# Kernel optimization log

Measured on AMD Instinct MI355X. Metric: run time of the kernel, lower is better.

The kernel has to match this reference:

```python
import jax, jax.numpy as jnp
import numpy as np

VOCAB = 100000
DIM = 128
BATCH = 65536
N_NEG = 10


def setup_inputs() -> dict:
    key = jax.random.key(0)
    k1, k2, k3, k4, k5 = jax.random.split(key, 5)
    return {
        "pos_u": jax.random.randint(k1, (BATCH,), 0, VOCAB),
        "pos_v": jax.random.randint(k2, (BATCH,), 0, VOCAB),
        "neg_v": jax.random.randint(k3, (BATCH, N_NEG), 0, VOCAB),
        "u_weight": 0.01 * jax.random.normal(k4, (VOCAB, DIM), dtype=jnp.float32),
        "v_weight": 0.01 * jax.random.normal(k5, (VOCAB, DIM), dtype=jnp.float32),
    }


def reference(pos_u, pos_v, neg_v, u_weight, v_weight):
    emb_u = u_weight[pos_u]            # [B, D]
    emb_v = v_weight[pos_v]            # [B, D]
    emb_neg_v = v_weight[neg_v]        # [B, N, D]

    score = jnp.sum(emb_u * emb_v, axis=1)
    score = jnp.clip(score, -10.0, 10.0)
    score = -jax.nn.log_sigmoid(score)           # [B]

    neg_dots = jnp.einsum("bd,bnd->bn", emb_u, emb_neg_v)  # [B, N]
    # NOTE: faithful to source: neg term is ADDED (not negated) to the loss
    neg_score = jnp.sum(jax.nn.log_sigmoid(-neg_dots), axis=1)  # [B]

    return jnp.mean(score + neg_score)
```

## Files before the change

### kernel.cpp

```cpp
#include <hip/hip_runtime.h>
#include <hip/hip_fp8.h>

#define VOCAB 100000
#define DIM 128
#define BATCH 65536
#define N_NEG 10

#define BLOCKS (BATCH / 32)
#define QSCALE 256.0f
#define QINV   (1.0f / (256.0f * 256.0f))

__device__ __forceinline__ unsigned int pack4_fp8(float a, float b, float c, float d) {
    unsigned int r =  (unsigned int)__hip_fp8_e4m3(a).__x;
    r |= (unsigned int)__hip_fp8_e4m3(b).__x << 8;
    r |= (unsigned int)__hip_fp8_e4m3(c).__x << 16;
    r |= (unsigned int)__hip_fp8_e4m3(d).__x << 24;
    return r;
}

__device__ __forceinline__ float fp8_to_f(unsigned int b) {
    __hip_fp8_e4m3 t; t.__x = (__hip_fp8_storage_t)b; return (float)t;
}

__device__ __forceinline__ float dot16_fp8(uint4 w, const float* uf) {
    float s = 0.0f;
    const unsigned int ws[4] = {w.x, w.y, w.z, w.w};
    #pragma unroll
    for (int q = 0; q < 4; ++q) {
        const unsigned int x = ws[q];
        s += uf[q * 4 + 0] * fp8_to_f(x & 0xffu);
        s += uf[q * 4 + 1] * fp8_to_f((x >> 8) & 0xffu);
        s += uf[q * 4 + 2] * fp8_to_f((x >> 16) & 0xffu);
        s += uf[q * 4 + 3] * fp8_to_f(x >> 24);
    }
    return s;
}

__device__ __forceinline__ float softplus_log2(float x) {
    const float y = x * 1.44269504f;
    const float t = __builtin_amdgcn_exp2f(-fabsf(y));
    return fmaxf(y, 0.0f) + __builtin_amdgcn_logf(1.0f + t);
}

__global__ void zero_out_kernel(float* out) { out[0] = 0.0f; }

__global__ __launch_bounds__(256) void quantize_kernel(
    const float4* __restrict__ in, uint4* __restrict__ out) {
    const int i = blockIdx.x * 256 + threadIdx.x;
    const float4 a = in[i * 4 + 0];
    const float4 b = in[i * 4 + 1];
    const float4 c = in[i * 4 + 2];
    const float4 d = in[i * 4 + 3];
    uint4 r;
    r.x = pack4_fp8(a.x * QSCALE, a.y * QSCALE, a.z * QSCALE, a.w * QSCALE);
    r.y = pack4_fp8(b.x * QSCALE, b.y * QSCALE, b.z * QSCALE, b.w * QSCALE);
    r.z = pack4_fp8(c.x * QSCALE, c.y * QSCALE, c.z * QSCALE, c.w * QSCALE);
    r.w = pack4_fp8(d.x * QSCALE, d.y * QSCALE, d.z * QSCALE, d.w * QSCALE);
    out[i] = r;
}

__global__ __launch_bounds__(256) void skipgram_loss_fp8_kernel(
    const int* __restrict__ pos_u,
    const int* __restrict__ pos_v,
    const int* __restrict__ neg_v,
    const uint4* __restrict__ u8,
    const uint4* __restrict__ v8,
    float* __restrict__ out)
{
    const int tid  = threadIdx.x;
    const int lane = tid & 63;
    const int wave = tid >> 6;
    const int sub  = lane & 7;
    const int grp  = lane >> 3;

    const int b = (blockIdx.x * 4 + wave) * 8 + grp;

    const int iu = pos_u[b];
    const int iv = pos_v[b];

    const uint4 uq = u8[iu * 8 + sub];
    float uf[16];
    {
        const unsigned int ws_[4] = {uq.x, uq.y, uq.z, uq.w};
        #pragma unroll
        for (int q = 0; q < 4; ++q) {
            uf[q * 4 + 0] = fp8_to_f(ws_[q] & 0xffu);
            uf[q * 4 + 1] = fp8_to_f((ws_[q] >> 8) & 0xffu);
            uf[q * 4 + 2] = fp8_to_f((ws_[q] >> 16) & 0xffu);
            uf[q * 4 + 3] = fp8_to_f(ws_[q] >> 24);
        }
    }

    float acc[N_NEG + 1];
    acc[0] = dot16_fp8(v8[iv * 8 + sub], uf);
    #pragma unroll
    for (int n = 0; n < N_NEG; ++n) {
        const int idx = neg_v[b * N_NEG + n];
        acc[n + 1] = dot16_fp8(v8[idx * 8 + sub], uf);
    }

    #pragma unroll
    for (int m = 1; m < 8; m <<= 1) {
        #pragma unroll
        for (int j = 0; j <= N_NEG; ++j) acc[j] += __shfl_xor(acc[j], m, 64);
    }

    float s = fminf(fmaxf(acc[0] * QINV, -10.0f), 10.0f);
    float loss2 = softplus_log2(-s);
    #pragma unroll
    for (int n = 0; n < N_NEG; ++n)
        loss2 -= softplus_log2(acc[n + 1] * QINV);
    float loss = loss2 * 0.69314718f;

    #pragma unroll
    for (int m = 8; m < 64; m <<= 1) loss += __shfl_xor(loss, m, 64);

    __shared__ float smem[4];
    if (lane == 0) smem[wave] = loss;
    __syncthreads();
    if (tid == 0)
        atomicAdd(out, (smem[0] + smem[1] + smem[2] + smem[3]) * (1.0f / (float)BATCH));
}

__device__ __forceinline__ float dot4(float4 a, float4 b) {
    return a.x * b.x + a.y * b.y + a.z * b.z + a.w * b.w;
}

__global__ __launch_bounds__(256) void skipgram_loss_fp32_kernel(
    const int* __restrict__ pos_u,
    const int* __restrict__ pos_v,
    const int* __restrict__ neg_v,
    const float4* __restrict__ u_weight,
    const float4* __restrict__ v_weight,
    float* __restrict__ out)
{
    const int tid  = threadIdx.x;
    const int lane = tid & 63;
    const int wave = tid >> 6;
    const int sub  = lane & 7;
    const int grp  = lane >> 3;

    const int b = (blockIdx.x * 4 + wave) * 8 + grp;

    const int iu = pos_u[b];
    const int iv = pos_v[b];

    const float4* __restrict__ urow = u_weight + iu * 32;
    float4 u0 = urow[0 * 8 + sub];
    float4 u1 = urow[1 * 8 + sub];
    float4 u2 = urow[2 * 8 + sub];
    float4 u3 = urow[3 * 8 + sub];

    const float4* __restrict__ vrow = v_weight + iv * 32;
    float p = dot4(u0, vrow[0 * 8 + sub]) + dot4(u1, vrow[1 * 8 + sub])
            + dot4(u2, vrow[2 * 8 + sub]) + dot4(u3, vrow[3 * 8 + sub]);

    float nd[N_NEG];
    #pragma unroll
    for (int n = 0; n < N_NEG; ++n) {
        const int idx = neg_v[b * N_NEG + n];
        const float4* __restrict__ wrow = v_weight + idx * 32;
        nd[n] = dot4(u0, wrow[0 * 8 + sub]) + dot4(u1, wrow[1 * 8 + sub])
              + dot4(u2, wrow[2 * 8 + sub]) + dot4(u3, wrow[3 * 8 + sub]);
    }

    #pragma unroll
    for (int m = 1; m < 8; m <<= 1) {
        p += __shfl_xor(p, m, 64);
        #pragma unroll
        for (int n = 0; n < N_NEG; ++n) nd[n] += __shfl_xor(nd[n], m, 64);
    }

    float s = fminf(fmaxf(p, -10.0f), 10.0f);
    float loss2 = softplus_log2(-s);
    #pragma unroll
    for (int n = 0; n < N_NEG; ++n) loss2 -= softplus_log2(nd[n]);
    float loss = loss2 * 0.69314718f;

    #pragma unroll
    for (int m = 8; m < 64; m <<= 1) loss += __shfl_xor(loss, m, 64);

    __shared__ float smem[4];
    if (lane == 0) smem[wave] = loss;
    __syncthreads();
    if (tid == 0)
        atomicAdd(out, (smem[0] + smem[1] + smem[2] + smem[3]) * (1.0f / (float)BATCH));
}

extern "C" void kernel_launch(void* const* d_in, const int* in_sizes, int n_in,
                              void* d_out, int out_size, void* d_ws, size_t ws_size,
                              hipStream_t stream) {
    const int*    pos_u    = (const int*)d_in[0];
    const int*    pos_v    = (const int*)d_in[1];
    const int*    neg_v    = (const int*)d_in[2];
    const float4* u_weight = (const float4*)d_in[3];
    const float4* v_weight = (const float4*)d_in[4];
    float* out = (float*)d_out;

    zero_out_kernel<<<1, 1, 0, stream>>>(out);

    const size_t table_bytes = (size_t)VOCAB * DIM;
    if (ws_size >= 2 * table_bytes) {
        uint4* u8 = (uint4*)d_ws;
        uint4* v8 = (uint4*)((char*)d_ws + table_bytes);
        const int qblocks = (VOCAB * DIM / 16) / 256;
        quantize_kernel<<<qblocks, 256, 0, stream>>>(u_weight, u8);
        quantize_kernel<<<qblocks, 256, 0, stream>>>(v_weight, v8);
        skipgram_loss_fp8_kernel<<<BLOCKS, 256, 0, stream>>>(
            pos_u, pos_v, neg_v, u8, v8, out);
    } else {
        skipgram_loss_fp32_kernel<<<BLOCKS, 256, 0, stream>>>(
            pos_u, pos_v, neg_v, u_weight, v_weight, out);
    }
}
```

Baseline: 170.3 us.

## Drop u-table quantization, read u rows in fp32, fuse output zeroing

Stops quantizing the u table to fp8 and instead reads the 65536 gathered u rows directly in fp32 inside the loss kernel, which removes one full-table quantize pass over 51 MB. Zeroing the output moves into the v quantize kernel, so one launch disappears. FP8 decode now uses the packed hardware convert builtin when it is available, which cuts per-element conversion instructions. The cost is 4x more bytes per u-row gather, but that is small next to reading the whole table.

```diff
diff --git a/kernel.cpp b/kernel.cpp
--- a/kernel.cpp
+++ b/kernel.cpp
@@ -8,7 +8,7 @@
 
 #define BLOCKS (BATCH / 32)
 #define QSCALE 256.0f
-#define QINV   (1.0f / (256.0f * 256.0f))
+#define QINV   (1.0f / 256.0f)
 
 __device__ __forceinline__ unsigned int pack4_fp8(float a, float b, float c, float d) {
     unsigned int r =  (unsigned int)__hip_fp8_e4m3(a).__x;
@@ -18,21 +18,29 @@
     return r;
 }
 
+#if __has_builtin(__builtin_amdgcn_cvt_pk_f32_fp8)
+typedef float v2f __attribute__((ext_vector_type(2)));
+__device__ __forceinline__ void fma4_fp8(float& s, unsigned int x, const float* u) {
+    v2f lo = __builtin_amdgcn_cvt_pk_f32_fp8(x, false);
+    v2f hi = __builtin_amdgcn_cvt_pk_f32_fp8(x, true);
+    s += u[0] * lo.x + u[1] * lo.y + u[2] * hi.x + u[3] * hi.y;
+}
+#else
 __device__ __forceinline__ float fp8_to_f(unsigned int b) {
     __hip_fp8_e4m3 t; t.__x = (__hip_fp8_storage_t)b; return (float)t;
 }
+__device__ __forceinline__ void fma4_fp8(float& s, unsigned int x, const float* u) {
+    s += u[0] * fp8_to_f(x & 0xffu) + u[1] * fp8_to_f((x >> 8) & 0xffu)
+       + u[2] * fp8_to_f((x >> 16) & 0xffu) + u[3] * fp8_to_f(x >> 24);
+}
+#endif
 
 __device__ __forceinline__ float dot16_fp8(uint4 w, const float* uf) {
     float s = 0.0f;
-    const unsigned int ws[4] = {w.x, w.y, w.z, w.w};
-    #pragma unroll
-    for (int q = 0; q < 4; ++q) {
-        const unsigned int x = ws[q];
-        s += uf[q * 4 + 0] * fp8_to_f(x & 0xffu);
-        s += uf[q * 4 + 1] * fp8_to_f((x >> 8) & 0xffu);
-        s += uf[q * 4 + 2] * fp8_to_f((x >> 16) & 0xffu);
-        s += uf[q * 4 + 3] * fp8_to_f(x >> 24);
-    }
+    fma4_fp8(s, w.x, uf + 0);
+    fma4_fp8(s, w.y, uf + 4);
+    fma4_fp8(s, w.z, uf + 8);
+    fma4_fp8(s, w.w, uf + 12);
     return s;
 }
 
@@ -44,9 +52,10 @@
 
 __global__ void zero_out_kernel(float* out) { out[0] = 0.0f; }
 
-__global__ __launch_bounds__(256) void quantize_kernel(
-    const float4* __restrict__ in, uint4* __restrict__ out) {
+__global__ __launch_bounds__(256) void quantize_v_kernel(
+    const float4* __restrict__ in, uint4* __restrict__ out, float* __restrict__ loss_out) {
     const int i = blockIdx.x * 256 + threadIdx.x;
+    if (i == 0) loss_out[0] = 0.0f;
     const float4 a = in[i * 4 + 0];
     const float4 b = in[i * 4 + 1];
     const float4 c = in[i * 4 + 2];
@@ -63,7 +72,7 @@
     const int* __restrict__ pos_u,
     const int* __restrict__ pos_v,
     const int* __restrict__ neg_v,
-    const uint4* __restrict__ u8,
+    const float4* __restrict__ u_weight,
     const uint4* __restrict__ v8,
     float* __restrict__ out)
 {
@@ -78,17 +87,13 @@
     const int iu = pos_u[b];
     const int iv = pos_v[b];
 
-    const uint4 uq = u8[iu * 8 + sub];
+    const float4* __restrict__ urow = u_weight + iu * 32 + sub * 4;
     float uf[16];
-    {
-        const unsigned int ws_[4] = {uq.x, uq.y, uq.z, uq.w};
-        #pragma unroll
-        for (int q = 0; q < 4; ++q) {
-            uf[q * 4 + 0] = fp8_to_f(ws_[q] & 0xffu);
-            uf[q * 4 + 1] = fp8_to_f((ws_[q] >> 8) & 0xffu);
-            uf[q * 4 + 2] = fp8_to_f((ws_[q] >> 16) & 0xffu);
-            uf[q * 4 + 3] = fp8_to_f(ws_[q] >> 24);
-        }
+    #pragma unroll
+    for (int q = 0; q < 4; ++q) {
+        const float4 t = urow[q];
+        uf[q * 4 + 0] = t.x; uf[q * 4 + 1] = t.y;
+        uf[q * 4 + 2] = t.z; uf[q * 4 + 3] = t.w;
     }
 
     float acc[N_NEG + 1];
@@ -197,18 +202,15 @@
     const float4* v_weight = (const float4*)d_in[4];
     float* out = (float*)d_out;
 
-    zero_out_kernel<<<1, 1, 0, stream>>>(out);
-
     const size_t table_bytes = (size_t)VOCAB * DIM;
-    if (ws_size >= 2 * table_bytes) {
-        uint4* u8 = (uint4*)d_ws;
-        uint4* v8 = (uint4*)((char*)d_ws + table_bytes);
+    if (ws_size >= table_bytes) {
+        uint4* v8 = (uint4*)d_ws;
         const int qblocks = (VOCAB * DIM / 16) / 256;
-        quantize_kernel<<<qblocks, 256, 0, stream>>>(u_weight, u8);
-        quantize_kernel<<<qblocks, 256, 0, stream>>>(v_weight, v8);
+        quantize_v_kernel<<<qblocks, 256, 0, stream>>>(v_weight, v8, out);
         skipgram_loss_fp8_kernel<<<BLOCKS, 256, 0, stream>>>(
-            pos_u, pos_v, neg_v, u8, v8, out);
+            pos_u, pos_v, neg_v, u_weight, v8, out);
     } else {
+        zero_out_kernel<<<1, 1, 0, stream>>>(out);
         skipgram_loss_fp32_kernel<<<BLOCKS, 256, 0, stream>>>(
             pos_u, pos_v, neg_v, u_weight, v_weight, out);
     }
```

Measured after the change: 151.6 us. 11.0% less time.
